# Kernel tuning notes

Measured on AMD Instinct MI355X. Metric: run time of the kernel, lower is better.

Reference implementation:

```python
import jax, jax.numpy as jnp
import numpy as np

T, N, C, L = 256, 64, 4096, 32
BLANK = 0
NEG = -1e30  # effective log(0)


def setup_inputs() -> dict:
    key = jax.random.key(0)
    k1, k2 = jax.random.split(key)
    preds = jax.random.normal(k1, (T, N, C), dtype=jnp.float32)
    # labels in [1, C): never equal to blank index 0
    targets = jax.random.randint(k2, (N * L,), 1, C, dtype=jnp.int32)
    pred_lengths = jnp.full((N,), T, dtype=jnp.int32)
    target_lengths = jnp.full((N,), L, dtype=jnp.int32)
    return {"preds": preds, "targets": targets,
            "pred_lengths": pred_lengths, "target_lengths": target_lengths}


def _ctc_loss(log_probs, targets2d, pred_lengths, target_lengths):
    # log_probs: (T, N, C); targets2d: (N, L)
    T_, N_, _ = log_probs.shape
    L_ = targets2d.shape[1]
    S = 2 * L_ + 1
    # extended label sequence: blank, l1, blank, l2, ..., blank  -> (N, S)
    ext = jnp.full((N_, S), BLANK, dtype=targets2d.dtype)
    ext = ext.at[:, 1::2].set(targets2d)
    # lp_ext[t, n, s] = log_probs[t, n, ext[n, s]]  -> (T, N, S)
    lp_ext = log_probs[:, jnp.arange(N_)[:, None], ext]
    s_idx = jnp.arange(S)
    # positions beyond this sample's extended length are invalid
    valid_s = s_idx[None, :] < (2 * target_lengths[:, None] + 1)  # (N, S)
    # skip (s-2 -> s) transition allowed only for non-blank labels that differ
    # from the label two positions back
    skip_ok = (s_idx[None, :] >= 2) & (ext != BLANK) & (ext != jnp.roll(ext, 2, axis=1))

    alpha0 = jnp.full((N_, S), NEG, dtype=log_probs.dtype)
    alpha0 = alpha0.at[:, 0].set(lp_ext[0, :, 0])
    alpha0 = alpha0.at[:, 1].set(jnp.where(target_lengths > 0, lp_ext[0, :, 1], NEG))
    alpha0 = jnp.where(valid_s, alpha0, NEG)

    def step(alpha, inp):
        lp_t, t = inp
        a1 = alpha
        a2 = jnp.concatenate([jnp.full((N_, 1), NEG, alpha.dtype), alpha[:, :-1]], axis=1)
        a3 = jnp.concatenate([jnp.full((N_, 2), NEG, alpha.dtype), alpha[:, :-2]], axis=1)
        a3 = jnp.where(skip_ok, a3, NEG)
        comb = jnp.logaddexp(jnp.logaddexp(a1, a2), a3)
        new = jnp.where(valid_s, comb + lp_t, NEG)
        active = (t < pred_lengths)[:, None]  # freeze alpha past sample end
        return jnp.where(active, new, alpha), None

    alphaT, _ = jax.lax.scan(step, alpha0, (lp_ext[1:], jnp.arange(1, T_)))
    end = 2 * target_lengths  # index of final blank in extended sequence
    a_last = jnp.take_along_axis(alphaT, end[:, None], axis=1)[:, 0]
    a_prev = jnp.take_along_axis(alphaT, jnp.maximum(end - 1, 0)[:, None], axis=1)[:, 0]
    a_prev = jnp.where(target_lengths > 0, a_prev, NEG)
    nll = -jnp.logaddexp(a_last, a_prev)
    # zero_infinity=True: zero out infinite / degenerate losses
    nll = jnp.where(jnp.isfinite(nll) & (nll < 1e29), nll, 0.0)
    # reduction='mean': divide each loss by its target length, then batch mean
    return jnp.mean(nll / jnp.maximum(target_lengths, 1).astype(nll.dtype))


def reference(preds, targets, pred_lengths, target_lengths):
    log_probs = jax.nn.log_softmax(preds, axis=2)
    targets2d = targets.reshape(N, L)  # all target_lengths equal L here
    return _ctc_loss(log_probs, targets2d, pred_lengths, target_lengths)
```

## Files before the change

kernel.cpp:

```cpp
#include <hip/hip_runtime.h>
#include <math.h>

#define T_ 256
#define N_ 64
#define C_ 4096
#define L_ 32
#define SL_ 33
#define NEGV (-1e30f)

__device__ __forceinline__ float lae2(float a, float b) {
    float m = fmaxf(a, b);
    return m + __logf(__expf(a - m) + __expf(b - m));
}

__device__ __forceinline__ float dpp_shr1(float x, float fill) {
    int r = __builtin_amdgcn_update_dpp(__float_as_int(fill), __float_as_int(x),
                                        0x138, 0xF, 0xF, false);
    return __int_as_float(r);
}

__device__ __forceinline__ float wred_max(float v) {
    #pragma unroll
    for (int o = 32; o > 0; o >>= 1) v = fmaxf(v, __shfl_xor(v, o));
    return v;
}
__device__ __forceinline__ float wred_sum(float v) {
    #pragma unroll
    for (int o = 32; o > 0; o >>= 1) v += __shfl_xor(v, o);
    return v;
}

__global__ __launch_bounds__(256) void k_row_lse(
        const float* __restrict__ preds, const int* __restrict__ targets,
        float* __restrict__ lp, int* __restrict__ counter) {
    const int wv     = threadIdx.x >> 6;
    const int lane   = threadIdx.x & 63;
    const int row_id = (blockIdx.x << 2) | wv;
    if (blockIdx.x == 0 && threadIdx.x == 0) *counter = 0;
    const int n = row_id & (N_ - 1);
    const float* row = preds + (size_t)row_id * C_;

    float gv = 0.f;
    if (lane < SL_) {
        const int cls = (lane == 0) ? 0 : targets[n * L_ + (lane - 1)];
        gv = row[cls];
    }

    float4 v[16];
    #pragma unroll
    for (int k = 0; k < 16; ++k) v[k] = ((const float4*)row)[lane + (k << 6)];

    float m = v[0].x;
    #pragma unroll
    for (int k = 0; k < 16; ++k)
        m = fmaxf(m, fmaxf(fmaxf(v[k].x, v[k].y), fmaxf(v[k].z, v[k].w)));
    m = wred_max(m);

    float s = 0.f;
    #pragma unroll
    for (int k = 0; k < 16; ++k)
        s += __expf(v[k].x - m) + __expf(v[k].y - m)
           + __expf(v[k].z - m) + __expf(v[k].w - m);
    s = wred_sum(s);
    const float lse = m + __logf(s);

    if (lane < SL_) {
        const int t = row_id >> 6;
        lp[((size_t)n * T_ + t) * SL_ + lane] = gv - lse;
    }
}

__global__ __launch_bounds__(256) void k_ctc_scan(
        const float* __restrict__ lp, const int* __restrict__ targets,
        const int* __restrict__ plen, const int* __restrict__ tlen,
        float* __restrict__ partial, int* __restrict__ counter,
        float* __restrict__ out) {
    __shared__ __align__(16) float lds[(T_ + 16) * SL_];
    const int n = blockIdx.x;
    const int tid = threadIdx.x;
    const float4* src = (const float4*)(lp + (size_t)n * T_ * SL_);
    float4* dst = (float4*)lds;
    for (int i = tid; i < (T_ * SL_) / 4; i += 256) dst[i] = src[i];
    __syncthreads();
    if (tid >= 64) return;

    const int lane = tid;
    const int tl = tlen[n];
    const int pl = plen[n];
    const int ends = 2 * tl;
    const bool odd = (lane & 1);
    const int slot   = odd ? 1 + (lane >> 1) : 0;
    const int cls    = odd ? targets[n * L_ + (lane >> 1)] : 0;
    const int clsm2  = (odd && lane >= 2) ? targets[n * L_ + (lane >> 1) - 1] : 0;
    const bool skip  = odd && (lane >= 2) && (cls != 0) && (cls != clsm2);
    const bool valid   = lane < 2 * tl + 1;
    const bool valid64 = (2 * tl + 1) > 64;

    float a = NEGV, b = NEGV;
    if (lane == 0) a = lds[0];
    if (lane == 1 && tl > 0) a = lds[1];

    float pf_s[4], pf_b[4];
    #pragma unroll
    for (int j = 0; j < 4; ++j) {
        pf_s[j] = lds[(1 + j) * SL_ + slot];
        pf_b[j] = lds[(1 + j) * SL_];
    }
    for (int t = 1; t <= T_; t += 4) {
        #pragma unroll
        for (int j = 0; j < 4; ++j) {
            const float lp_s = pf_s[j];
            const float lp64 = pf_b[j];
            pf_s[j] = lds[(t + 4 + j) * SL_ + slot];
            pf_b[j] = lds[(t + 4 + j) * SL_];

            const float a2 = dpp_shr1(a, NEGV);
            float a3 = dpp_shr1(a2, NEGV);
            a3 = skip ? a3 : NEGV;
            const float m3 = fmaxf(fmaxf(a, a2), a3);
            const float comb = m3 + __logf(__expf(a - m3) + __expf(a2 - m3)
                                           + __expf(a3 - m3));
            const float nb = valid64 ? (lae2(b, a) + lp64) : NEGV;
            const float na = valid ? (comb + lp_s) : NEGV;
            const int tt = t + j;
            if (tt < pl) { a = na; b = nb; }
        }
    }

    const float a_last = (ends >= 64) ? __shfl(b, 63) : __shfl(a, ends);
    float a_prev = __shfl(a, (ends > 0) ? (ends - 1) : 0);
    if (tl <= 0) a_prev = NEGV;
    float nll = -lae2(a_last, a_prev);
    if (!(isfinite(nll) && nll < 1e29f)) nll = 0.f;
    if (lane == 0) partial[n] = nll / (float)((tl > 0) ? tl : 1);

    __threadfence();
    int done = 0;
    if (lane == 0) done = atomicAdd(counter, 1);
    done = __shfl(done, 0);
    if (done == N_ - 1) {
        __threadfence();
        float v = partial[lane];
        v = wred_sum(v);
        if (lane == 0) out[0] = v * (1.0f / (float)N_);
    }
}

extern "C" void kernel_launch(void* const* d_in, const int* in_sizes, int n_in,
                              void* d_out, int out_size, void* d_ws, size_t ws_size,
                              hipStream_t stream) {
    const float* preds   = (const float*)d_in[0];
    const int*   targets = (const int*)d_in[1];
    const int*   plen    = (const int*)d_in[2];
    const int*   tlen    = (const int*)d_in[3];

    float* lp      = (float*)d_ws;
    float* partial = lp + (size_t)N_ * T_ * SL_;
    int*   counter = (int*)(partial + N_);

    k_row_lse<<<(T_ * N_) / 4, 256, 0, stream>>>(preds, targets, lp, counter);
    k_ctc_scan<<<N_, 256, 0, stream>>>(lp, targets, plen, tlen, partial,
                                       counter, (float*)d_out);
}
```

Before: 406.6 us.

## Run CTC alpha recursion in scaled probability space instead of log space

```diff
diff --git a/kernel.cpp b/kernel.cpp
--- a/kernel.cpp
+++ b/kernel.cpp
@@ -7,11 +7,6 @@
 #define L_ 32
 #define SL_ 33
 #define NEGV (-1e30f)
-
-__device__ __forceinline__ float lae2(float a, float b) {
-    float m = fmaxf(a, b);
-    return m + __logf(__expf(a - m) + __expf(b - m));
-}
 
 __device__ __forceinline__ float dpp_shr1(float x, float fill) {
     int r = __builtin_amdgcn_update_dpp(__float_as_int(fill), __float_as_int(x),
@@ -32,7 +27,7 @@
 
 __global__ __launch_bounds__(256) void k_row_lse(
         const float* __restrict__ preds, const int* __restrict__ targets,
-        float* __restrict__ lp, int* __restrict__ counter) {
+        float* __restrict__ pmat, int* __restrict__ counter) {
     const int wv     = threadIdx.x >> 6;
     const int lane   = threadIdx.x & 63;
     const int row_id = (blockIdx.x << 2) | wv;
@@ -66,19 +61,19 @@
 
     if (lane < SL_) {
         const int t = row_id >> 6;
-        lp[((size_t)n * T_ + t) * SL_ + lane] = gv - lse;
+        pmat[((size_t)n * T_ + t) * SL_ + lane] = __expf(gv - lse);
     }
 }
 
 __global__ __launch_bounds__(256) void k_ctc_scan(
-        const float* __restrict__ lp, const int* __restrict__ targets,
+        const float* __restrict__ pmat, const int* __restrict__ targets,
         const int* __restrict__ plen, const int* __restrict__ tlen,
         float* __restrict__ partial, int* __restrict__ counter,
         float* __restrict__ out) {
     __shared__ __align__(16) float lds[(T_ + 16) * SL_];
     const int n = blockIdx.x;
     const int tid = threadIdx.x;
-    const float4* src = (const float4*)(lp + (size_t)n * T_ * SL_);
+    const float4* src = (const float4*)(pmat + (size_t)n * T_ * SL_);
     float4* dst = (float4*)lds;
     for (int i = tid; i < (T_ * SL_) / 4; i += 256) dst[i] = src[i];
     __syncthreads();
@@ -96,9 +91,10 @@
     const bool valid   = lane < 2 * tl + 1;
     const bool valid64 = (2 * tl + 1) > 64;
 
-    float a = NEGV, b = NEGV;
-    if (lane == 0) a = lds[0];
-    if (lane == 1 && tl > 0) a = lds[1];
+    float A = 0.f, B = 0.f;
+    float Slog = 0.f;
+    if (lane == 0) A = lds[0];
+    if (lane == 1 && tl > 0) A = lds[1];
 
     float pf_s[4], pf_b[4];
     #pragma unroll
@@ -106,31 +102,38 @@
         pf_s[j] = lds[(1 + j) * SL_ + slot];
         pf_b[j] = lds[(1 + j) * SL_];
     }
+
     for (int t = 1; t <= T_; t += 4) {
         #pragma unroll
         for (int j = 0; j < 4; ++j) {
-            const float lp_s = pf_s[j];
-            const float lp64 = pf_b[j];
+            const float p_s = pf_s[j];
+            const float p_b = pf_b[j];
             pf_s[j] = lds[(t + 4 + j) * SL_ + slot];
             pf_b[j] = lds[(t + 4 + j) * SL_];
 
-            const float a2 = dpp_shr1(a, NEGV);
-            float a3 = dpp_shr1(a2, NEGV);
-            a3 = skip ? a3 : NEGV;
-            const float m3 = fmaxf(fmaxf(a, a2), a3);
-            const float comb = m3 + __logf(__expf(a - m3) + __expf(a2 - m3)
-                                           + __expf(a3 - m3));
-            const float nb = valid64 ? (lae2(b, a) + lp64) : NEGV;
-            const float na = valid ? (comb + lp_s) : NEGV;
-            const int tt = t + j;
-            if (tt < pl) { a = na; b = nb; }
+            const float A2 = dpp_shr1(A, 0.f);
+            float A3 = dpp_shr1(A2, 0.f);
+            A3 = skip ? A3 : 0.f;
+            const float sum3 = (A + A2) + A3;
+            const float nA = valid ? sum3 * p_s : 0.f;
+            const float nB = valid64 ? (B + A) * p_b : 0.f;
+            if (t + j < pl) { A = nA; B = nB; }
+        }
+        if (t + 3 < pl) {
+            float mx = fmaxf(A, (lane == 63) ? B : 0.f);
+            mx = wred_max(mx);
+            if (mx > 0.f) {
+                const float inv = 1.0f / mx;
+                A *= inv; B *= inv;
+                Slog += __logf(mx);
+            }
         }
     }
 
-    const float a_last = (ends >= 64) ? __shfl(b, 63) : __shfl(a, ends);
-    float a_prev = __shfl(a, (ends > 0) ? (ends - 1) : 0);
-    if (tl <= 0) a_prev = NEGV;
-    float nll = -lae2(a_last, a_prev);
+    const float a_last = (ends >= 64) ? __shfl(B, 63) : __shfl(A, ends);
+    float a_prev = __shfl(A, (ends > 0) ? (ends - 1) : 0);
+    if (tl <= 0) a_prev = 0.f;
+    float nll = -(__logf(a_last + a_prev) + Slog);
     if (!(isfinite(nll) && nll < 1e29f)) nll = 0.f;
     if (lane == 0) partial[n] = nll / (float)((tl > 0) ? tl : 1);
 
@@ -154,11 +157,11 @@
     const int*   plen    = (const int*)d_in[2];
     const int*   tlen    = (const int*)d_in[3];
 
-    float* lp      = (float*)d_ws;
-    float* partial = lp + (size_t)N_ * T_ * SL_;
+    float* pmat    = (float*)d_ws;
+    float* partial = pmat + (size_t)N_ * T_ * SL_;
     int*   counter = (int*)(partial + N_);
 
-    k_row_lse<<<(T_ * N_) / 4, 256, 0, stream>>>(preds, targets, lp, counter);
-    k_ctc_scan<<<N_, 256, 0, stream>>>(lp, targets, plen, tlen, partial,
+    k_row_lse<<<(T_ * N_) / 4, 256, 0, stream>>>(preds, targets, pmat, counter);
+    k_ctc_scan<<<N_, 256, 0, stream>>>(pmat, targets, plen, tlen, partial,
                                        counter, (float*)d_out);
 }
```

Measured after the change: 393.3 us. -3.3%, faster.
